# Kernel tuning notes

Measured on AMD Instinct MI355X. Metric: run time of the kernel, lower is better.

Reference implementation:

```python
import jax, jax.numpy as jnp
import numpy as np
from jax import lax

DN = ('NDHWC', 'DHWIO', 'NDHWC')
SHAPE = (33, 33, 33)
B = 2
N = 40000
C = 64


def setup_inputs() -> dict:
    key = jax.random.key(0)
    ks = jax.random.split(key, 24)
    D, H, W = SHAPE
    # unique active voxel coords (batch, z, y, x)
    rng = np.random.default_rng(0)
    idx = rng.choice(B * D * H * W, size=N, replace=False)
    b = idx // (D * H * W)
    r = idx % (D * H * W)
    coors = np.stack([b, r // (H * W), (r // W) % H, r % W], axis=1).astype(np.int32)

    def w(k, shape, scale=0.1):
        return jax.random.normal(k, shape, jnp.float32) * scale

    inp = {
        'features': jax.random.normal(ks[0], (N, 3), jnp.float32),
        'coors': jnp.asarray(coors),
        'batch_size': B,
        'w1': w(ks[1], (3, 3, 3, 3, C), 0.2), 'b1': w(ks[2], (C,), 0.05),
        'w2': w(ks[3], (3, 3, 3, C, C), 0.05), 'b2': w(ks[4], (C,), 0.05),
        'w3': w(ks[5], (3, 3, 3, C, C), 0.05), 'b3': w(ks[6], (C,), 0.05),
        'wt': w(ks[7], (3, 3, 3, C, C), 0.05), 'bt': w(ks[8], (C,), 0.05),
        'w5': w(ks[9], (3, 3, 3, C, C), 0.05), 'b5': w(ks[10], (C,), 0.05),
    }
    # folded eval-mode BatchNorm: y = x*s + h  (s = gamma/sqrt(var+eps), h = beta - mean*s)
    for i, (sk, hk) in enumerate(zip(ks[11:16], ks[16:21]), start=1):
        inp[f's{i}'] = 1.0 + 0.1 * jax.random.normal(sk, (C,), jnp.float32)
        inp[f'h{i}'] = 0.05 * jax.random.normal(hk, (C,), jnp.float32)
    return inp


def _forward(features, coors, batch_size,
             w1, b1, w2, b2, w3, b3, wt, bt, w5, b5,
             s1, h1, s2, h2, s3, h3, s4, h4, s5, h5):
    D, H, W = SHAPE
    bi, zi, yi, xi = coors[:, 0], coors[:, 1], coors[:, 2], coors[:, 3]
    # densify SparseConvTensor (zeros at inactive sites) + active mask
    x = jnp.zeros((batch_size, D, H, W, features.shape[-1]), features.dtype)
    x = x.at[bi, zi, yi, xi].set(features)
    m = jnp.zeros((batch_size, D, H, W, 1), jnp.float32).at[bi, zi, yi, xi].set(1.0)
    ones3 = jnp.ones((3, 3, 3, 1, 1), jnp.float32)

    conv = lambda a, k, pad: lax.conv_general_dilated(a, k, (1, 1, 1), pad, dimension_numbers=DN)
    # masked BN(eval) + ReLU: applied only on active sites, background stays exactly 0
    act = lambda y, mm, s, h: jnp.where(mm, jax.nn.relu(y * s + h), 0.0)

    # SparseConv3d(3,64,3): valid conv; output actives = 1-dilation of input actives
    x = conv(x, w1, 'VALID')
    m1 = conv(m, ones3, 'VALID') > 0  # [B,31,31,31,1]
    x = act(x + b1, m1, s1, h1)

    # two SubMConv3d(64,64,3) sharing indice_key: same active set, SAME padding
    x = act(conv(x, w2, 'SAME') + b2, m1, s2, h2)
    x = act(conv(x, w3, 'SAME') + b3, m1, s3, h3)

    # SparseConvTranspose3d(64,64,3,2): out = (D-1)*2+3; actives = transposed dilation
    x = lax.conv_transpose(x, wt, (2, 2, 2), 'VALID', dimension_numbers=DN)
    mT = lax.conv_transpose(m1.astype(jnp.float32), ones3, (2, 2, 2), 'VALID', dimension_numbers=DN) > 0
    x = act(x + bt, mT, s4, h4)

    # ToDense -> dense Conv3d(64,64,3) -> BN -> ReLU (dense: applied everywhere)
    x = conv(x, w5, 'VALID') + b5
    x = jax.nn.relu(x * s5 + h5)
    return jnp.transpose(x, (0, 4, 1, 2, 3))  # NCDHW like spconv ToDense output


def reference(features, coors, batch_size,
              w1, b1, w2, b2, w3, b3, wt, bt, w5, b5,
              s1, h1, s2, h2, s3, h3, s4, h4, s5, h5):
    return _forward(features, coors, batch_size,
                    w1, b1, w2, b2, w3, b3, wt, bt, w5, b5,
                    s1, h1, s2, h2, s3, h3, s4, h4, s5, h5)
```

## Files before the change

### kernel.cpp

```cpp
#include <hip/hip_runtime.h>
#include <cstdint>

constexpr int BB = 2, C = 64;
constexpr int D1 = 31;
constexpr int DP = 33;
constexpr int D4 = 63;
constexpr int D5 = 61;
constexpr int D5CUBE = D5*D5*D5;

constexpr int NV1 = BB*D1*D1*D1;
constexpr int NVP = BB*DP*DP*DP;
constexpr int NV4 = BB*D4*D4*D4;
constexpr int NV5 = BB*D5*D5*D5;

constexpr size_t alup(size_t x) { return (x + 255) & ~(size_t)255; }
constexpr size_t OB_X0  = 0;
constexpr size_t OB_M0  = alup(OB_X0  + (size_t)NVP*3*4);
constexpr size_t OB_M1P = alup(OB_M0  + (size_t)NVP*4);
constexpr size_t OB_X1  = alup(OB_M1P + (size_t)NVP*4);
constexpr size_t OB_X2  = alup(OB_X1  + (size_t)NVP*64*2);
constexpr size_t OB_X3  = alup(OB_X2  + (size_t)NVP*64*2);
constexpr size_t OB_MT  = alup(OB_X3  + (size_t)NVP*64*2);
constexpr size_t OB_X4  = alup(OB_MT  + (size_t)NV4*4);
constexpr size_t OB_WB2 = alup(OB_X4  + (size_t)NV4*64*2);
constexpr size_t OB_WB3 = alup(OB_WB2 + (size_t)27*64*64*2);
constexpr size_t OB_WBT = alup(OB_WB3 + (size_t)27*64*64*2);
constexpr size_t OB_WB5 = alup(OB_WBT + (size_t)27*64*64*2);

typedef __attribute__((ext_vector_type(8))) short short8;
typedef __attribute__((ext_vector_type(4))) float f32x4;

__device__ inline unsigned short f2bf(float f) {
  unsigned int u = __float_as_uint(f);
  u = (u + 0x7FFFu + ((u >> 16) & 1u)) >> 16;
  return (unsigned short)u;
}

template<int DD>
__device__ inline void decodev(int vox, int& b, int& z, int& y, int& x) {
  x = vox % DD; int r = vox / DD;
  y = r % DD;   r /= DD;
  z = r % DD;   b = r / DD;
}

__device__ inline int xcd_swz(int bid, int nb) {
  int q = nb >> 3, r = nb & 7;
  int xcd = bid & 7, idx = bid >> 3;
  return (xcd < r ? xcd*(q+1) : r*(q+1) + (xcd - r)*q) + idx;
}

__global__ void __launch_bounds__(256)
k_zero(float* __restrict__ x0, float* __restrict__ m0, float* __restrict__ m1p,
       unsigned short* __restrict__ x1, unsigned short* __restrict__ x2,
       unsigned short* __restrict__ x3) {
  int v = blockIdx.x*256 + threadIdx.x;
  if (v >= NVP) return;
  m0[v] = 0.f; m1p[v] = 0.f;
  x0[3*v+0] = 0.f; x0[3*v+1] = 0.f; x0[3*v+2] = 0.f;
  int x = v % DP, r = v / DP;
  int y = r % DP; r /= DP;
  int z = r % DP;
  if (x==0 || x==DP-1 || y==0 || y==DP-1 || z==0 || z==DP-1) {
    ulonglong2 zz = {0ull, 0ull};
    ulonglong2* p1 = (ulonglong2*)(x1 + (size_t)v*64);
    ulonglong2* p2 = (ulonglong2*)(x2 + (size_t)v*64);
    ulonglong2* p3 = (ulonglong2*)(x3 + (size_t)v*64);
    #pragma unroll
    for (int i = 0; i < 8; i++) { p1[i] = zz; p2[i] = zz; p3[i] = zz; }
  }
}

__global__ void k_scatter(const float* __restrict__ feat, const int* __restrict__ coors,
                          int n, float* __restrict__ x0, float* __restrict__ m0) {
  int i = blockIdx.x*blockDim.x + threadIdx.x;
  if (i >= n) return;
  int b = coors[4*i+0], z = coors[4*i+1], y = coors[4*i+2], x = coors[4*i+3];
  int v = ((b*DP + z)*DP + y)*DP + x;
  x0[v*3+0] = feat[3*i+0];
  x0[v*3+1] = feat[3*i+1];
  x0[v*3+2] = feat[3*i+2];
  m0[v] = 1.0f;
}

__global__ void __launch_bounds__(256)
k_conv1(const float* __restrict__ x0, const float* __restrict__ m0,
        unsigned short* __restrict__ x1, float* __restrict__ m1p,
        const float* __restrict__ w1, const float* __restrict__ b1,
        const float* __restrict__ s1, const float* __restrict__ h1) {
  long long t = (long long)blockIdx.x*blockDim.x + threadIdx.x;
  if (t >= (long long)NV1*C) return;
  int co  = (int)(t & 63);
  int vox = (int)(t >> 6);
  int b, z, y, x; decodev<D1>(vox, b, z, y, x);
  float sum = 0.f, mm = 0.f;
  #pragma unroll
  for (int kz=0; kz<3; kz++)
  #pragma unroll
  for (int ky=0; ky<3; ky++)
  #pragma unroll
  for (int kx=0; kx<3; kx++) {
    int iv = ((b*DP + z+kz)*DP + y+ky)*DP + (x+kx);
    mm += m0[iv];
    const float* px = x0 + iv*3;
    const float* pw = w1 + ((kz*3+ky)*3+kx)*3*64 + co;
    sum += px[0]*pw[0] + px[1]*pw[64] + px[2]*pw[128];
  }
  bool m = mm > 0.f;
  float o = m ? fmaxf((sum + b1[co])*s1[co] + h1[co], 0.f) : 0.f;
  size_t pOff = (size_t)(((b*DP + z+1)*DP + y+1)*DP + (x+1));
  x1[pOff*C + co] = f2bf(o);
  if (co == 0) m1p[pOff] = m ? 1.f : 0.f;
}

__global__ void k_repack4(const float* __restrict__ wa, const float* __restrict__ wb,
                          const float* __restrict__ wc, const float* __restrict__ wd,
                          unsigned short* __restrict__ da, unsigned short* __restrict__ db,
                          unsigned short* __restrict__ dc, unsigned short* __restrict__ dd) {
  int which = blockIdx.x / 432;
  int i = (blockIdx.x - which*432)*256 + threadIdx.x;
  const float* w = which == 0 ? wa : which == 1 ? wb : which == 2 ? wc : wd;
  unsigned short* dst = which == 0 ? da : which == 1 ? db : which == 2 ? dc : dd;
  int co = i & 63, k = (i >> 6) & 63, t = i >> 12;
  int kk = k >> 5, q = (k >> 3) & 3, j = k & 7, cb = co >> 4, l = q*16 + (co & 15);
  dst[(size_t)((t*2+kk)*4+cb)*512 + l*8 + j] = f2bf(w[i]);
}

__global__ void __launch_bounds__(256)
k_maskT(const float* __restrict__ m1p, float* __restrict__ mt) {
  int vox = blockIdx.x*256 + threadIdx.x;
  if (vox >= NV4) return;
  int b, zo, yo, xo; decodev<D4>(vox, b, zo, yo, xo);
  float mm = 0.f;
  for (int kz = 0; kz < 3; kz++) {
    if ((zo + kz) & 1) continue;
    int izp = ((zo + kz - 2) >> 1) + 1;
    for (int ky = 0; ky < 3; ky++) {
      if ((yo + ky) & 1) continue;
      int iyp = ((yo + ky - 2) >> 1) + 1;
      for (int kx = 0; kx < 3; kx++) {
        if ((xo + kx) & 1) continue;
        int ixp = ((xo + kx - 2) >> 1) + 1;
        mm += m1p[((b*DP + izp)*DP + iyp)*DP + ixp];
      }
    }
  }
  mt[vox] = mm;
}

__device__ __forceinline__ void c_step2(const short8 (&A)[2], const short8 (&W)[4],
                                        f32x4 (&acc)[2][4]) {
  #pragma unroll
  for (int a = 0; a < 2; a++)
    #pragma unroll
    for (int cb = 0; cb < 4; cb++)
      acc[a][cb] = __builtin_amdgcn_mfma_f32_16x16x32_bf16(W[cb], A[a], acc[a][cb], 0, 0, 0);
}

__device__ __forceinline__ void c5_step(const short8 (&A)[4], const short8 (&W)[4],
                                        f32x4 (&acc)[4][4]) {
  #pragma unroll
  for (int a = 0; a < 4; a++)
    #pragma unroll
    for (int cb = 0; cb < 4; cb++)
      acc[a][cb] = __builtin_amdgcn_mfma_f32_16x16x32_bf16(W[cb], A[a], acc[a][cb], 0, 0, 0);
}

constexpr int C23_HALF = 1280;

__global__ void __launch_bounds__(256)
k_conv23_mfma(const unsigned short* __restrict__ xin, const unsigned short* __restrict__ wB,
              unsigned short* __restrict__ xout, const float* __restrict__ m1p,
              const float* __restrict__ bias, const float* __restrict__ s,
              const float* __restrict__ h) {
  __shared__ short8 sA[2*C23_HALF];
  const int tid  = threadIdx.x;
  const int lane = tid & 63;
  const int wid  = tid >> 6;
  const int ll   = lane & 15;
  const int l16  = lane >> 4;

  const int blk = xcd_swz(blockIdx.x, gridDim.x);
  const int yt  = blk & 7;
  const int rzb = blk >> 3;
  const int z   = rzb % D1;
  const int b   = rzb / D1;
  const int y0  = yt * 4;

  int st_r[5], st_base[5];
  #pragma unroll
  for (int it = 0; it < 5; ++it) {
    int g = it*256 + tid; g = g > 1055 ? 1055 : g;
    int r = g / 264, rem = g - r*264;
    int v = rem >> 3, c16p = rem & 7;
    int c16l = c16p ^ (v & 7);
    st_r[it] = r;
    st_base[it] = (v << 7) + (c16l << 4);
  }

  const char* xinb = (const char*)xin;

  f32x4 acc[2][4];
  #pragma unroll
  for (int a = 0; a < 2; a++)
    #pragma unroll
    for (int cb = 0; cb < 4; cb++)
      acc[a][cb] = f32x4{0.f, 0.f, 0.f, 0.f};

  auto STAGE = [&](int kzn, int kyn, int hn) {
    size_t pb = (size_t)((b*DP + z + kzn)*DP) * (DP*128);
    char* dst = (char*)&sA[0] + hn*(C23_HALF*16);
    #pragma unroll
    for (int it = 0; it < 5; ++it) {
      int yin = y0 + st_r[it] + kyn; yin = yin > 32 ? 32 : yin;
      __builtin_amdgcn_global_load_lds(
        (const __attribute__((address_space(1))) void*)(xinb + pb + (size_t)yin*(DP*128) + st_base[it]),
        (__attribute__((address_space(3))) void*)(dst + it*4096 + wid*1024),
        16, 0, 0);
    }
  };
  auto LDA = [&](int hh, int kx, int kk, short8 (&A)[2]) {
    #pragma unroll
    for (int a = 0; a < 2; a++) {
      int xv = a*16 + ll; xv = xv > 30 ? 30 : xv;
      int v  = xv + kx;
      int ch = hh*C23_HALF + wid*264 + v*8 + ((kk*4 + l16) ^ (v & 7));
      A[a] = sA[ch];
    }
  };

  short8 A0[2], A1[2];

  STAGE(0, 0, 0);
  __syncthreads();

  int kzn = 0, kyn = 1;
  #pragma unroll 1
  for (int p = 0; p < 9; ++p) {
    const int hh = p & 1;

    short8 W[6][4];
    {
      const unsigned short* wp = wB + (size_t)p*12288 + lane*8;
      #pragma unroll
      for (int st = 0; st < 6; ++st)
        #pragma unroll
        for (int cb = 0; cb < 4; cb++)
          W[st][cb] = *reinterpret_cast<const short8*>(wp + st*2048 + cb*512);
    }
    __builtin_amdgcn_sched_barrier(0);

    if (p < 8) {
      STAGE(kzn, kyn, hh ^ 1);
      kyn++; if (kyn == 3) { kyn = 0; kzn++; }
    }
    __builtin_amdgcn_sched_barrier(0);

    LDA(hh, 0, 0, A0);
    #pragma unroll
    for (int st = 0; st < 6; ++st) {
      const int kxn = (st+1) >> 1, kkn = (st+1) & 1;
      if (st < 5) {
        if (st & 1) LDA(hh, kxn, kkn, A0); else LDA(hh, kxn, kkn, A1);
      }
      if (st & 1) c_step2(A1, W[st], acc); else c_step2(A0, W[st], acc);
    }
    __syncthreads();
  }

  const int y = y0 + wid;
  if (y < D1) {
    #pragma unroll
    for (int a = 0; a < 2; a++) {
      int x = a*16 + ll;
      if (x >= D1) continue;
      size_t pOff = (size_t)(((b*DP + z+1)*DP + y+1)*DP + (x+1));
      bool m = m1p[pOff] > 0.f;
      #pragma unroll
      for (int cb = 0; cb < 4; cb++) {
        unsigned long long pack = 0;
        #pragma unroll
        for (int r = 0; r < 4; r++) {
          int co = cb*16 + l16*4 + r;
          float o = m ? fmaxf((acc[a][cb][r] + bias[co])*s[co] + h[co], 0.f) : 0.f;
          pack |= (unsigned long long)f2bf(o) << (16*r);
        }
        *reinterpret_cast<unsigned long long*>(xout + pOff*64 + cb*16 + l16*4) = pack;
      }
    }
  }
}

constexpr int CT_CHUNKS = 1792;

__global__ void __launch_bounds__(256)
k_convT_mfma(const unsigned short* __restrict__ x3, const unsigned short* __restrict__ wB,
             unsigned short* __restrict__ x4, const float* __restrict__ mt,
             const float* __restrict__ bias, const float* __restrict__ s,
             const float* __restrict__ h) {
  __shared__ short8 sb[CT_CHUNKS];
  const int tid  = threadIdx.x;
  const int lane = tid & 63;
  const int wid  = tid >> 6;
  const int ii   = lane & 15;
  const int l16  = lane >> 4;

  const int blk   = xcd_swz(blockIdx.x, gridDim.x);
  const int ytile = blk & 15;
  const int rzb   = blk >> 4;
  const int zo    = rzb % D4;
  const int b     = rzb / D4;
  const int y0    = ytile * 4;

  const int izp0 = (zo + (zo & 1)) >> 1;
  const int izp1 = (zo & 1) ? izp0 : izp0 + 1;

  #pragma unroll
  for (int it = 0; it < 7; ++it) {
    int g = it*256 + tid; g = g > 1583 ? 1583 : g;
    int r6 = g / 264, rem = g - r6*264;
    int v = rem >> 3, c16p = rem & 7;
    int c16l = c16p ^ (v & 7);
    int pz  = r6 >= 3 ? 1 : 0;
    int ry  = r6 - pz*3;
    int izp = pz ? izp1 : izp0;
    int iyp = ytile*2 + ry;
    size_t srcB = ((size_t)((b*DP + izp)*DP + iyp)*DP)*128 + (size_t)(v << 7) + (c16l << 4);
    __builtin_amdgcn_global_load_lds(
      (const __attribute__((address_space(1))) void*)((const char*)x3 + srcB),
      (__attribute__((address_space(3))) void*)((char*)&sb[0] + it*4096 + wid*1024),
      16, 0, 0);
  }
  __syncthreads();

  f32x4 acc[4][4];
  #pragma unroll
  for (int a = 0; a < 4; a++)
    #pragma unroll
    for (int cb = 0; cb < 4; cb++)
      acc[a][cb] = f32x4{0.f, 0.f, 0.f, 0.f};

  const int yo = y0 + wid;
  if (yo < D4) {
    const int nPz = (zo & 1) ? 1 : 2;
    #pragma unroll 1
    for (int pz = 0; pz < 2; ++pz) {
      if (pz >= nPz) break;
      const int kz = (zo & 1) ? 1 : pz*2;
      #pragma unroll 1
      for (int kyi = 0; kyi < 2; ++kyi) {
        int ky, ry;
        if (wid & 1) { if (kyi == 1) break; ky = 1; ry = (wid + 1) >> 1; }
        else         { ky = kyi*2;          ry = (wid >> 1) + kyi; }
        const int rbase = (pz*3 + ry)*264;
        #pragma unroll
        for (int kx = 0; kx < 3; ++kx) {
          const int apar  = kx & 1;
          const int xoffE = ((kx + apar - 2) >> 1) + 1;
          const int t = (kz*3 + ky)*3 + kx;
          #pragma unroll
          for (int kk = 0; kk < 2; ++kk) {
            short8 Bv[4];
            const unsigned short* wpk = wB + (size_t)(t*2+kk)*2048 + lane*8;
            #pragma unroll
            for (int cb = 0; cb < 4; cb++)
              Bv[cb] = *reinterpret_cast<const short8*>(wpk + cb*512);
            #pragma unroll
            for (int ablk = 0; ablk < 2; ablk++) {
              const int ixp = ablk*16 + ii + xoffE;
              short8 A = sb[rbase + ixp*8 + ((kk*4 + l16) ^ (ixp & 7))];
              const int afr = apar*2 + ablk;
              #pragma unroll
              for (int cb = 0; cb < 4; cb++)
                acc[afr][cb] = __builtin_amdgcn_mfma_f32_16x16x32_bf16(A, Bv[cb], acc[afr][cb], 0, 0, 0);
            }
          }
        }
      }
    }

    float bv[4], sv[4], hv[4];
    #pragma unroll
    for (int cb = 0; cb < 4; cb++) {
      int c = cb*16 + (lane & 15);
      bv[cb] = bias[c]; sv[cb] = s[c]; hv[cb] = h[c];
    }
    const int rowBase = ((b*D4 + zo)*D4 + yo)*D4;
    #pragma unroll
    for (int a = 0; a < 4; a++) {
      const int ablk = a & 1, apar = a >> 1;
      #pragma unroll
      for (int r = 0; r < 4; r++) {
        const int row = (lane >> 4)*4 + r;
        const int xo  = 2*(ablk*16 + row) + apar;
        if (xo >= D4) continue;
        const int vox = rowBase + xo;
        const bool m = mt[vox] > 0.f;
        #pragma unroll
        for (int cb = 0; cb < 4; cb++) {
          float o = m ? fmaxf((acc[a][cb][r] + bv[cb])*sv[cb] + hv[cb], 0.f) : 0.f;
          x4[(size_t)vox*64 + cb*16 + (lane & 15)] = f2bf(o);
        }
      }
    }
  }
}

__global__ void __launch_bounds__(256, 2)
k_conv5_mfma(const unsigned short* __restrict__ x4, const unsigned short* __restrict__ wB,
             float* __restrict__ out, const float* __restrict__ bias,
             const float* __restrict__ s, const float* __restrict__ h) {
  __shared__ short8 sA[2][2048];
  const int tid  = threadIdx.x;
  const int lane = tid & 63;
  const int wid  = tid >> 6;
  const int ll   = lane & 15;
  const int l16  = lane >> 4;

  const int blk   = xcd_swz(blockIdx.x, gridDim.x);
  const int ytile = blk & 15;
  const int rzb   = blk >> 4;
  const int z     = rzb % D5;
  const int b     = rzb / D5;
  const int y0    = ytile * 4;

  int st_r[8], st_base[8];
  #pragma unroll
  for (int it = 0; it < 8; ++it) {
    int g = it*256 + tid; g = g > 2015 ? 2015 : g;
    int r = g / 504, rem = g - r*504;
    int v = rem >> 3, c16p = rem & 7;
    int c16l = c16p ^ (v & 7);
    st_r[it] = r;
    st_base[it] = (v << 7) + (c16l << 4);
  }

  const char* x4b = (const char*)x4;

  f32x4 acc[4][4];
  #pragma unroll
  for (int a = 0; a < 4; a++)
    #pragma unroll
    for (int cb = 0; cb < 4; cb++)
      acc[a][cb] = f32x4{0.f, 0.f, 0.f, 0.f};

  auto STAGE_A = [&](int kzn, int kyn, int hn) {
    size_t pb = (size_t)(b*D4 + z + kzn) * (D4*D4*128);
    char* dst = (char*)&sA[hn][0];
    #pragma unroll
    for (int it = 0; it < 8; ++it) {
      int yin = y0 + st_r[it] + kyn; yin = yin > 62 ? 62 : yin;
      __builtin_amdgcn_global_load_lds(
        (const __attribute__((address_space(1))) void*)(x4b + pb + (size_t)yin*8064 + st_base[it]),
        (__attribute__((address_space(3))) void*)(dst + it*4096 + wid*1024),
        16, 0, 0);
    }
  };
  auto LDA = [&](int hh, int kx, int kk, short8 (&A)[4]) {
    #pragma unroll
    for (int a = 0; a < 4; a++) {
      int v  = a*16 + ll + kx;
      int ch = wid*504 + v*8 + ((kk*4 + l16) ^ (v & 7));
      A[a] = sA[hh][ch];
    }
  };

  short8 A0[4], A1[4], A2[4];

  STAGE_A(0, 0, 0);
  __syncthreads();

#define C5_BODY(p0,p1,p2,p3,p4,p5)                                    \
  do {                                                                 \
    LDA(hh, (p0)>>1, (p0)&1, A0);                                      \
    LDA(hh, (p1)>>1, (p1)&1, A1);                                      \
    LDA(hh, (p2)>>1, (p2)&1, A2);  c5_step(A0, W[p0], acc);            \
    LDA(hh, (p3)>>1, (p3)&1, A0);  c5_step(A1, W[p1], acc);            \
    LDA(hh, (p4)>>1, (p4)&1, A1);  c5_step(A2, W[p2], acc);            \
    LDA(hh, (p5)>>1, (p5)&1, A2);  c5_step(A0, W[p3], acc);            \
    c5_step(A1, W[p4], acc);                                           \
    c5_step(A2, W[p5], acc);                                           \
  } while (0)

  int kzn = 0, kyn = 1;
  #pragma unroll 1
  for (int p = 0; p < 9; ++p) {
    const int hh = p & 1;

    short8 W[6][4];
    {
      const unsigned short* wp = wB + (size_t)p*12288 + lane*8;
      #pragma unroll
      for (int st = 0; st < 6; ++st)
        #pragma unroll
        for (int cb = 0; cb < 4; cb++)
          W[st][cb] = *reinterpret_cast<const short8*>(wp + st*2048 + cb*512);
    }
    __builtin_amdgcn_sched_barrier(0);

    if (p < 8) {
      STAGE_A(kzn, kyn, hh ^ 1);
      kyn++; if (kyn == 3) { kyn = 0; kzn++; }
    }
    __builtin_amdgcn_sched_barrier(0);

    if ((wid & 1) == 0) {
      C5_BODY(0,1,2,3,4,5);
    } else {
      C5_BODY(3,4,5,0,1,2);
    }
    __syncthreads();
  }
#undef C5_BODY

  const int yout = y0 + wid;
  if (yout < D5) {
    #pragma unroll
    for (int a = 0; a < 4; a++) {
      int x = a*16 + ll;
      if (x >= D5) continue;
      size_t sp = (size_t)(z*D5 + yout)*D5 + x;
      #pragma unroll
      for (int cb = 0; cb < 4; cb++)
        #pragma unroll
        for (int r = 0; r < 4; r++) {
          int co = cb*16 + l16*4 + r;
          float o = fmaxf((acc[a][cb][r] + bias[co])*s[co] + h[co], 0.f);
          out[(size_t)(b*64 + co)*D5CUBE + sp] = o;
        }
    }
  }
}

extern "C" void kernel_launch(void* const* d_in, const int* in_sizes, int n_in,
                              void* d_out, int out_size, void* d_ws, size_t ws_size,
                              hipStream_t stream) {
  const float* feat  = (const float*)d_in[0];
  const int*   coors = (const int*)d_in[1];
  const float* w1 = (const float*)d_in[3];
  const float* b1 = (const float*)d_in[4];
  const float* w2 = (const float*)d_in[5];
  const float* b2 = (const float*)d_in[6];
  const float* w3 = (const float*)d_in[7];
  const float* b3 = (const float*)d_in[8];
  const float* wt = (const float*)d_in[9];
  const float* bt = (const float*)d_in[10];
  const float* w5 = (const float*)d_in[11];
  const float* b5 = (const float*)d_in[12];
  const float* s1 = (const float*)d_in[13];
  const float* h1 = (const float*)d_in[14];
  const float* s2 = (const float*)d_in[15];
  const float* h2 = (const float*)d_in[16];
  const float* s3 = (const float*)d_in[17];
  const float* h3 = (const float*)d_in[18];
  const float* s4 = (const float*)d_in[19];
  const float* h4 = (const float*)d_in[20];
  const float* s5 = (const float*)d_in[21];
  const float* h5 = (const float*)d_in[22];
  int n = in_sizes[0] / 3;

  char* wsb = (char*)d_ws;
  float*          X0  = (float*)(wsb + OB_X0);
  float*          M0  = (float*)(wsb + OB_M0);
  float*          M1P = (float*)(wsb + OB_M1P);
  unsigned short* X1  = (unsigned short*)(wsb + OB_X1);
  unsigned short* X2  = (unsigned short*)(wsb + OB_X2);
  unsigned short* X3  = (unsigned short*)(wsb + OB_X3);
  float*          MT  = (float*)(wsb + OB_MT);
  unsigned short* X4  = (unsigned short*)(wsb + OB_X4);
  unsigned short* WB2 = (unsigned short*)(wsb + OB_WB2);
  unsigned short* WB3 = (unsigned short*)(wsb + OB_WB3);
  unsigned short* WBT = (unsigned short*)(wsb + OB_WBT);
  unsigned short* WB5 = (unsigned short*)(wsb + OB_WB5);

  k_zero<<<(NVP + 255)/256, 256, 0, stream>>>(X0, M0, M1P, X1, X2, X3);

  k_repack4<<<1728, 256, 0, stream>>>(w2, w3, wt, w5, WB2, WB3, WBT, WB5);

  k_scatter<<<(n+255)/256, 256, 0, stream>>>(feat, coors, n, X0, M0);

  {
    long long threads = (long long)NV1*C;
    k_conv1<<<(int)((threads+255)/256), 256, 0, stream>>>(X0, M0, X1, M1P, w1, b1, s1, h1);
  }

  constexpr int BLK23 = BB * D1 * 8;
  k_conv23_mfma<<<BLK23, 256, 0, stream>>>(X1, WB2, X2, M1P, b2, s2, h2);
  k_conv23_mfma<<<BLK23, 256, 0, stream>>>(X2, WB3, X3, M1P, b3, s3, h3);

  k_maskT<<<(NV4 + 255)/256, 256, 0, stream>>>(M1P, MT);

  constexpr int BLK_T = BB * D4 * 16;
  k_convT_mfma<<<BLK_T, 256, 0, stream>>>(X3, WBT, X4, MT, bt, s4, h4);

  constexpr int BLK5 = BB * D5 * 16;
  k_conv5_mfma<<<BLK5, 256, 0, stream>>>(X4, WB5, (float*)d_out, b5, s5, h5);
}
```

Baseline: 321.2 us.

## Make conv5 LDS staging per-wave and replace block barriers with vmcnt waits

Each wave now stages only its own input row into a private LDS slot (padded to 544 entries) instead of the block staging all four rows cooperatively. Because no wave reads another wave's data, the per-iteration __syncthreads is replaced by an s_waitcnt vmcnt(8) that waits only for the previous stage's loads. A dummy stage is issued on the last iteration so the vmcnt count stays constant, and the staggered weight-step order across waves is dropped. This removes block-wide barrier stalls, but relies on per-wave ordering of global_load_lds completion with no LDS-side wait.

```diff
diff --git a/kernel.cpp b/kernel.cpp
--- a/kernel.cpp
+++ b/kernel.cpp
@@ -405,11 +405,13 @@
   }
 }
 
+constexpr int C5_WSLOT = 544;
+
 __global__ void __launch_bounds__(256, 2)
 k_conv5_mfma(const unsigned short* __restrict__ x4, const unsigned short* __restrict__ wB,
              float* __restrict__ out, const float* __restrict__ bias,
              const float* __restrict__ s, const float* __restrict__ h) {
-  __shared__ short8 sA[2][2048];
+  __shared__ short8 sA[2*4*C5_WSLOT];
   const int tid  = threadIdx.x;
   const int lane = tid & 63;
   const int wid  = tid >> 6;
@@ -423,15 +425,13 @@
   const int b     = rzb / D5;
   const int y0    = ytile * 4;
 
-  int st_r[8], st_base[8];
+  int st_off[8];
   #pragma unroll
   for (int it = 0; it < 8; ++it) {
-    int g = it*256 + tid; g = g > 2015 ? 2015 : g;
-    int r = g / 504, rem = g - r*504;
-    int v = rem >> 3, c16p = rem & 7;
+    int g = it*64 + lane; g = g > 503 ? 503 : g;
+    int v = g >> 3, c16p = g & 7;
     int c16l = c16p ^ (v & 7);
-    st_r[it] = r;
-    st_base[it] = (v << 7) + (c16l << 4);
+    st_off[it] = (v << 7) + (c16l << 4);
   }
 
   const char* x4b = (const char*)x4;
@@ -443,15 +443,15 @@
     for (int cb = 0; cb < 4; cb++)
       acc[a][cb] = f32x4{0.f, 0.f, 0.f, 0.f};
 
-  auto STAGE_A = [&](int kzn, int kyn, int hn) {
-    size_t pb = (size_t)(b*D4 + z + kzn) * (D4*D4*128);
-    char* dst = (char*)&sA[hn][0];
+  auto STAGE = [&](int kzn, int kyn, int hn) {
+    int yin = y0 + wid + kyn; yin = yin > 62 ? 62 : yin;
+    size_t rb = ((size_t)((b*D4 + z + kzn)*D4 + yin)) * 8064;
+    char* dst = (char*)&sA[0] + (size_t)(hn*4 + wid)*(C5_WSLOT*16);
     #pragma unroll
     for (int it = 0; it < 8; ++it) {
-      int yin = y0 + st_r[it] + kyn; yin = yin > 62 ? 62 : yin;
       __builtin_amdgcn_global_load_lds(
-        (const __attribute__((address_space(1))) void*)(x4b + pb + (size_t)yin*8064 + st_base[it]),
-        (__attribute__((address_space(3))) void*)(dst + it*4096 + wid*1024),
+        (const __attribute__((address_space(1))) void*)(x4b + rb + st_off[it]),
+        (__attribute__((address_space(3))) void*)(dst + it*1024),
         16, 0, 0);
     }
   };
@@ -459,15 +459,14 @@
     #pragma unroll
     for (int a = 0; a < 4; a++) {
       int v  = a*16 + ll + kx;
-      int ch = wid*504 + v*8 + ((kk*4 + l16) ^ (v & 7));
-      A[a] = sA[hh][ch];
+      int ch = (hh*4 + wid)*C5_WSLOT + v*8 + ((kk*4 + l16) ^ (v & 7));
+      A[a] = sA[ch];
     }
   };
 
   short8 A0[4], A1[4], A2[4];
 
-  STAGE_A(0, 0, 0);
-  __syncthreads();
+  STAGE(0, 0, 0);
 
 #define C5_BODY(p0,p1,p2,p3,p4,p5)                                    \
   do {                                                                 \
@@ -498,17 +497,17 @@
     __builtin_amdgcn_sched_barrier(0);
 
     if (p < 8) {
-      STAGE_A(kzn, kyn, hh ^ 1);
+      STAGE(kzn, kyn, hh ^ 1);
       kyn++; if (kyn == 3) { kyn = 0; kzn++; }
+    } else {
+      STAGE(2, 2, hh ^ 1);
     }
     __builtin_amdgcn_sched_barrier(0);
 
-    if ((wid & 1) == 0) {
-      C5_BODY(0,1,2,3,4,5);
-    } else {
-      C5_BODY(3,4,5,0,1,2);
-    }
-    __syncthreads();
+    asm volatile("s_waitcnt vmcnt(8)" ::: "memory");
+    __builtin_amdgcn_sched_barrier(0);
+
+    C5_BODY(0,1,2,3,4,5);
   }
 #undef C5_BODY
 
```

After: 319.9 us. No clear change (-0.4%).
